# Kernel tuning notes

Hardware: AMD Instinct MI355X
Metric: run time of the kernel (lower is better)

## Reference

```python
import jax, jax.numpy as jnp
import numpy as np

MESH_SIZE = 0.01
TEMP = 0.001
T = 4096
HID = (16, 16, 16)


def _triangle_mesh():
    g = np.arange(-1.0, 1.0 + 1e-9, MESH_SIZE, dtype=np.float32)  # 201 pts
    A, B = np.meshgrid(g, g, indexing='ij')  # alpha rows, beta cols
    mask = A >= B                             # Preisach triangle alpha >= beta
    return A[mask].astype(np.float32), B[mask].astype(np.float32)  # [N], [N]


def _constrain(v, lo, hi):
    return lo + (hi - lo) * jax.nn.sigmoid(v)


def setup_inputs() -> dict:
    key = jax.random.key(0)
    ks = jax.random.split(key, 12)
    alpha_np, beta_np = _triangle_mesh()
    N = alpha_np.shape[0]  # 20301

    def xavier(k, fan_in, fan_out):
        b = np.sqrt(6.0 / (fan_in + fan_out)).astype(np.float32)
        return jax.random.uniform(k, (fan_in, fan_out), jnp.float32, -b, b)

    dims = (2,) + HID + (1,)
    params = {}
    for i in range(4):
        params[f'w{i+1}'] = xavier(ks[i], dims[i], dims[i + 1])
        params[f'b{i+1}'] = jnp.zeros((dims[i + 1],), jnp.float32)

    bound = np.sqrt(6.0 / (1 + N)).astype(np.float32)  # xavier_uniform on (1,N)
    init_state_raw = jax.random.uniform(ks[10], (N,), jnp.float32, -bound, bound)

    return dict(
        x=jax.random.normal(ks[11], (T,), jnp.float32),
        alpha_raw=jnp.asarray(alpha_np),
        beta_raw=jnp.asarray(beta_np),
        init_state_raw=init_state_raw,
        m_scale_raw=jnp.asarray(1.0, jnp.float32),
        m_offset_raw=jnp.asarray(1.0, jnp.float32),
        h_scale_raw=jnp.asarray(1.0, jnp.float32),
        **params,
    )


def _get_states(x, alpha, beta, s0, temp):
    # Soft Preisach relay: switch up where u>alpha, down where u<beta, else hold.
    def step(s, u):
        up = jax.nn.sigmoid((u - alpha) / temp)
        dn = jax.nn.sigmoid((beta - u) / temp)
        s_new = up - dn + (1.0 - up) * (1.0 - dn) * s
        return s_new, s_new
    _, states = jax.lax.scan(step, s0, x)
    return states  # [T, N]


def reference(x, alpha_raw, beta_raw, init_state_raw,
              w1, b1, w2, b2, w3, b3, w4, b4,
              m_scale_raw, m_offset_raw, h_scale_raw):
    alpha = alpha_raw  # ConstrainedParameter with no bounds -> identity
    beta = beta_raw
    s0 = jnp.tanh(init_state_raw)  # BinaryParameter (soft binary)

    states = _get_states(x, alpha, beta, s0, TEMP)  # [T, N]

    mesh = jnp.stack([alpha, beta], axis=1)  # [N, 2]
    h = jax.nn.relu(mesh @ w1 + b1)
    h = jax.nn.relu(h @ w2 + b2)
    h = jax.nn.relu(h @ w3 + b3)
    density = jax.nn.sigmoid(h @ w4 + b4)  # [N, 1]
    density = density.T  # [1, N]

    m = jnp.sum(density * states, axis=-1) / jnp.sum(density, axis=-1)  # [T]

    m_scale = _constrain(m_scale_raw, 0.0, 10.0)
    m_offset = _constrain(m_offset_raw, -10.0, 10.0)
    h_scale = _constrain(h_scale_raw, 0.0, 10.0)

    out = m_scale * m + m_offset + h_scale * x  # [T]
    return out, density, states
```

## Files before the change

kernel.cpp:

```cpp
#include <hip/hip_runtime.h>
#include <math.h>

#define NM 20301
#define TT 4096
#define NC 64
#define CH 64
#define NBLK 80
#define SBLK 20
#define NPROW (SBLK * 4)
#define TPH 16
#define NPH (CH / TPH)
#define LOG2E_K 1442.69504f
#define WNEAR 26.0f

__device__ __forceinline__ void relay_step(float ka, float kb, float ku,
                                           float& aa, float& bb) {
    float z1 = fminf(ka - ku, 63.f);
    float z2 = fminf(ku - kb, 63.f);
    float e1 = __builtin_amdgcn_exp2f(z1);
    float e2 = __builtin_amdgcn_exp2f(z2);
    float p1 = 1.f + e1, p2 = 1.f + e2;
    float r  = __builtin_amdgcn_rcpf(p1 * p2);
    aa = (e2 - e1) * r;
    bb = (e1 * e2) * r;
}

__device__ __forceinline__ float wave_reduce_sum(float w) {
    #pragma unroll
    for (int off = 32; off > 0; off >>= 1)
        w += __shfl_down(w, off, 64);
    return w;
}

__global__ __launch_bounds__(256) void density_kernel(
    const float* __restrict__ alpha, const float* __restrict__ beta,
    const float* __restrict__ w1, const float* __restrict__ b1,
    const float* __restrict__ w2, const float* __restrict__ b2,
    const float* __restrict__ w3, const float* __restrict__ b3,
    const float* __restrict__ w4, const float* __restrict__ b4,
    float* __restrict__ density_out, float* __restrict__ densum_parts)
{
    int n = blockIdx.x * 256 + threadIdx.x;
    bool valid = n < NM;
    int nn = valid ? n : NM - 1;
    float a = alpha[nn], b = beta[nn];

    float h1[16], h2[16], h3[16];
    #pragma unroll
    for (int j = 0; j < 16; j++) {
        float v = fmaf(a, w1[j], fmaf(b, w1[16 + j], b1[j]));
        h1[j] = fmaxf(v, 0.f);
    }
    #pragma unroll
    for (int j = 0; j < 16; j++) {
        float v = b2[j];
        #pragma unroll
        for (int k = 0; k < 16; k++) v = fmaf(h1[k], w2[k * 16 + j], v);
        h2[j] = fmaxf(v, 0.f);
    }
    #pragma unroll
    for (int j = 0; j < 16; j++) {
        float v = b3[j];
        #pragma unroll
        for (int k = 0; k < 16; k++) v = fmaf(h2[k], w3[k * 16 + j], v);
        h3[j] = fmaxf(v, 0.f);
    }
    float v = b4[0];
    #pragma unroll
    for (int k = 0; k < 16; k++) v = fmaf(h3[k], w4[k], v);
    float d = 1.f / (1.f + __expf(-v));

    if (valid) density_out[n] = d;
    float wsum = wave_reduce_sum(valid ? d : 0.f);
    __shared__ float ws_[4];
    if ((threadIdx.x & 63) == 0) ws_[threadIdx.x >> 6] = wsum;
    __syncthreads();
    if (threadIdx.x == 0)
        densum_parts[blockIdx.x] = ws_[0] + ws_[1] + ws_[2] + ws_[3];
}

__global__ __launch_bounds__(256) void chunk_compose_kernel(
    const float* __restrict__ x, const float* __restrict__ alpha,
    const float* __restrict__ beta,
    float* __restrict__ Abuf, float* __restrict__ Bbuf)
{
    __shared__ float xs[CH];
    int c = blockIdx.y;
    if (threadIdx.x < CH) xs[threadIdx.x] = x[c * CH + threadIdx.x] * LOG2E_K;
    __syncthreads();

    int n = blockIdx.x * 256 + threadIdx.x;
    int nn = (n < NM) ? n : NM - 1;
    float ka = alpha[nn] * LOG2E_K;
    float kb = beta[nn] * LOG2E_K;

    float A = 0.f, B = 1.f;
    for (int p = 0; p < NPH; p++) {
        float xr[TPH];
        #pragma unroll
        for (int j = 0; j < TPH; j++) xr[j] = xs[p * TPH + j];
        #pragma unroll
        for (int j = 0; j < TPH; j++) {
            float ku = xr[j];
            float d1 = ka - ku, d2 = ku - kb;
            bool nearb = fminf(fabsf(d1), fabsf(d2)) < WNEAR;
            if (__any(nearb)) {
                float aa, bb;
                relay_step(ka, kb, ku, aa, bb);
                A = fmaf(bb, A, aa);
                B *= bb;
            } else {
                bool su = d1 < 0.f, sd = d2 < 0.f;
                A = su ? 1.f : (sd ? -1.f : A);
                B = (su || sd) ? 0.f : B;
            }
        }
    }
    if (n < NM) { Abuf[(size_t)c * NM + n] = A; Bbuf[(size_t)c * NM + n] = B; }
}

__global__ __launch_bounds__(256) void chunk_scan_kernel(
    const float* __restrict__ init_raw,
    const float* __restrict__ Abuf, const float* __restrict__ Bbuf,
    float* __restrict__ sstart)
{
    int n = blockIdx.x * 256 + threadIdx.x;
    if (n >= NM) return;
    float s = tanhf(init_raw[n]);
    #pragma unroll 4
    for (int c = 0; c < NC; c++) {
        sstart[(size_t)c * NM + n] = s;
        s = fmaf(Bbuf[(size_t)c * NM + n], s, Abuf[(size_t)c * NM + n]);
    }
}

__global__ __launch_bounds__(256) void states_kernel(
    const float* __restrict__ x, const float* __restrict__ alpha,
    const float* __restrict__ beta, const float* __restrict__ density,
    const float* __restrict__ sstart,
    float* __restrict__ states, float* __restrict__ partials)
{
    __shared__ float xs[CH];
    __shared__ float tile[4 * 64 * (TPH + 1)];

    int tid = threadIdx.x;
    int c = blockIdx.y;
    if (tid < CH) xs[tid] = x[c * CH + tid] * LOG2E_K;

    int n0 = blockIdx.x * 1024 + tid;
    float s[4], d[4], ka[4], kb[4];
    bool v[4];
    #pragma unroll
    for (int q = 0; q < 4; q++) {
        int n = n0 + q * 256;
        v[q] = n < NM;
        int nn = v[q] ? n : NM - 1;
        ka[q] = alpha[nn] * LOG2E_K;
        kb[q] = beta[nn] * LOG2E_K;
        d[q]  = v[q] ? density[n] : 0.f;
        s[q]  = sstart[(size_t)c * NM + nn];
    }
    __syncthreads();

    int wv = tid >> 6, ln = tid & 63;
    int tl = ln & 15, h = ln >> 4;
    float* wtile = &tile[wv * 64 * (TPH + 1)];
    float* tslot = &wtile[ln * (TPH + 1)];
    float* rp    = states + (size_t)c * CH * NM + n0;
    size_t prow  = (size_t)(blockIdx.x * 4 + wv) * TT + c * CH;

    for (int p = 0; p < NPH; p++) {
        float xr[TPH];
        #pragma unroll
        for (int j = 0; j < TPH; j++) xr[j] = xs[p * TPH + j];
        #pragma unroll
        for (int j = 0; j < TPH; j++) {
            float u = xr[j];
            float w1_[4], w2_[4], nr[4];
            #pragma unroll
            for (int q = 0; q < 4; q++) {
                w1_[q] = ka[q] - u;
                w2_[q] = u - kb[q];
                nr[q]  = fminf(fabsf(w1_[q]), fabsf(w2_[q]));
            }
            float nmin = fminf(fminf(nr[0], nr[1]), fminf(nr[2], nr[3]));
            if (__any(nmin < WNEAR)) {
                #pragma unroll
                for (int q = 0; q < 4; q++) {
                    float aa, bb;
                    relay_step(ka[q], kb[q], u, aa, bb);
                    s[q] = fmaf(bb, s[q], aa);
                }
            } else {
                #pragma unroll
                for (int q = 0; q < 4; q++)
                    s[q] = (w1_[q] < 0.f) ? 1.f
                         : ((w2_[q] < 0.f) ? -1.f : s[q]);
            }
            #pragma unroll
            for (int q = 0; q < 4; q++)
                if (v[q]) rp[q * 256] = s[q];
            rp += NM;
            tslot[j] = fmaf(d[0], s[0], fmaf(d[1], s[1],
                       fmaf(d[2], s[2], d[3] * s[3])));
        }
        asm volatile("s_waitcnt lgkmcnt(0)" ::: "memory");
        float acc = 0.f;
        #pragma unroll
        for (int k = 0; k < TPH; k++)
            acc += wtile[(h * 16 + k) * (TPH + 1) + tl];
        acc += __shfl_xor(acc, 16, 64);
        acc += __shfl_xor(acc, 32, 64);
        if (ln < TPH) partials[prow + p * TPH + ln] = acc;
        asm volatile("s_waitcnt lgkmcnt(0)" ::: "memory");
    }
}

__global__ __launch_bounds__(256) void finalize_kernel(
    const float* __restrict__ x, const float* __restrict__ partials,
    const float* __restrict__ densum_parts,
    const float* __restrict__ msr, const float* __restrict__ mor,
    const float* __restrict__ hsr, float* __restrict__ out)
{
    int t = blockIdx.x * 256 + threadIdx.x;
    if (t >= TT) return;
    float acc = 0.f;
    for (int r = 0; r < NPROW; r++)
        acc += partials[(size_t)r * TT + t];
    float dsum = 0.f;
    for (int bx = 0; bx < NBLK; bx++)
        dsum += densum_parts[bx];
    float sig_ms = 1.f / (1.f + __expf(-msr[0]));
    float sig_mo = 1.f / (1.f + __expf(-mor[0]));
    float sig_hs = 1.f / (1.f + __expf(-hsr[0]));
    float m_scale  = 10.f * sig_ms;
    float m_offset = fmaf(20.f, sig_mo, -10.f);
    float h_scale  = 10.f * sig_hs;
    float m = acc / dsum;
    out[t] = fmaf(m_scale, m, m_offset) + h_scale * x[t];
}

extern "C" void kernel_launch(void* const* d_in, const int* in_sizes, int n_in,
                              void* d_out, int out_size, void* d_ws, size_t ws_size,
                              hipStream_t stream)
{
    const float* x    = (const float*)d_in[0];
    const float* alpha= (const float*)d_in[1];
    const float* beta = (const float*)d_in[2];
    const float* init = (const float*)d_in[3];
    const float* msr  = (const float*)d_in[4];
    const float* mor  = (const float*)d_in[5];
    const float* hsr  = (const float*)d_in[6];
    const float* w1   = (const float*)d_in[7];
    const float* b1   = (const float*)d_in[8];
    const float* w2   = (const float*)d_in[9];
    const float* b2   = (const float*)d_in[10];
    const float* w3   = (const float*)d_in[11];
    const float* b3   = (const float*)d_in[12];
    const float* w4   = (const float*)d_in[13];
    const float* b4   = (const float*)d_in[14];

    float* out     = (float*)d_out;
    float* density = out + TT;
    float* states  = density + NM;

    float* densum_parts = (float*)d_ws;
    float* sstart       = densum_parts + 128;
    float* partials     = sstart + (size_t)NC * NM;

    float* Abuf = states;
    float* Bbuf = states + (size_t)NC * NM;

    density_kernel<<<dim3(NBLK), dim3(256), 0, stream>>>(
        alpha, beta, w1, b1, w2, b2, w3, b3, w4, b4, density, densum_parts);

    chunk_compose_kernel<<<dim3(NBLK, NC), dim3(256), 0, stream>>>(
        x, alpha, beta, Abuf, Bbuf);

    chunk_scan_kernel<<<dim3(NBLK), dim3(256), 0, stream>>>(
        init, Abuf, Bbuf, sstart);

    states_kernel<<<dim3(SBLK, NC), dim3(256), 0, stream>>>(
        x, alpha, beta, density, sstart, states, partials);

    finalize_kernel<<<dim3(TT / 256), dim3(256), 0, stream>>>(
        x, partials, densum_parts, msr, mor, hsr, out);
}
```

Before: 452.9 us.

## Fuse chunk compose, scan and states into one decoupled-lookback kernel

Replaces the three-pass chunked scan (compose, sequential chunk scan, states replay) with a single kernel. Each block first computes its chunk's affine composition assuming a zero start and writes those provisional states. It then publishes A/B via release flags and looks back over earlier chunks, stopping early once the composed multiplier becomes zero. A final fix-up pass rewrites states only while the start state still matters and adds density-weighted corrections into an extra partials row. This removes one full relay-step pass over all timesteps and the sstart round trip. In exchange it adds spin-waiting on inter-block flags, with a recompute fallback after a timeout, plus extra shared-memory atomics.

```diff
diff --git a/kernel.cpp b/kernel.cpp
--- a/kernel.cpp
+++ b/kernel.cpp
@@ -8,8 +8,10 @@
 #define NBLK 80
 #define SBLK 20
 #define NPROW (SBLK * 4)
+#define NROWS (NPROW + SBLK)
 #define TPH 16
 #define NPH (CH / TPH)
+#define NFLAGS (NC * SBLK)
 #define LOG2E_K 1442.69504f
 #define WNEAR 26.0f
 
@@ -38,9 +40,11 @@
     const float* __restrict__ w2, const float* __restrict__ b2,
     const float* __restrict__ w3, const float* __restrict__ b3,
     const float* __restrict__ w4, const float* __restrict__ b4,
-    float* __restrict__ density_out, float* __restrict__ densum_parts)
+    float* __restrict__ density_out, float* __restrict__ densum_parts,
+    int* __restrict__ flags)
 {
     int n = blockIdx.x * 256 + threadIdx.x;
+    if (n < NFLAGS) flags[n] = 0;
     bool valid = n < NM;
     int nn = valid ? n : NM - 1;
     float a = alpha[nn], b = beta[nn];
@@ -79,76 +83,24 @@
         densum_parts[blockIdx.x] = ws_[0] + ws_[1] + ws_[2] + ws_[3];
 }
 
-__global__ __launch_bounds__(256) void chunk_compose_kernel(
-    const float* __restrict__ x, const float* __restrict__ alpha,
-    const float* __restrict__ beta,
-    float* __restrict__ Abuf, float* __restrict__ Bbuf)
-{
-    __shared__ float xs[CH];
-    int c = blockIdx.y;
-    if (threadIdx.x < CH) xs[threadIdx.x] = x[c * CH + threadIdx.x] * LOG2E_K;
-    __syncthreads();
-
-    int n = blockIdx.x * 256 + threadIdx.x;
-    int nn = (n < NM) ? n : NM - 1;
-    float ka = alpha[nn] * LOG2E_K;
-    float kb = beta[nn] * LOG2E_K;
-
-    float A = 0.f, B = 1.f;
-    for (int p = 0; p < NPH; p++) {
-        float xr[TPH];
-        #pragma unroll
-        for (int j = 0; j < TPH; j++) xr[j] = xs[p * TPH + j];
-        #pragma unroll
-        for (int j = 0; j < TPH; j++) {
-            float ku = xr[j];
-            float d1 = ka - ku, d2 = ku - kb;
-            bool nearb = fminf(fabsf(d1), fabsf(d2)) < WNEAR;
-            if (__any(nearb)) {
-                float aa, bb;
-                relay_step(ka, kb, ku, aa, bb);
-                A = fmaf(bb, A, aa);
-                B *= bb;
-            } else {
-                bool su = d1 < 0.f, sd = d2 < 0.f;
-                A = su ? 1.f : (sd ? -1.f : A);
-                B = (su || sd) ? 0.f : B;
-            }
-        }
-    }
-    if (n < NM) { Abuf[(size_t)c * NM + n] = A; Bbuf[(size_t)c * NM + n] = B; }
-}
-
-__global__ __launch_bounds__(256) void chunk_scan_kernel(
-    const float* __restrict__ init_raw,
-    const float* __restrict__ Abuf, const float* __restrict__ Bbuf,
-    float* __restrict__ sstart)
-{
-    int n = blockIdx.x * 256 + threadIdx.x;
-    if (n >= NM) return;
-    float s = tanhf(init_raw[n]);
-    #pragma unroll 4
-    for (int c = 0; c < NC; c++) {
-        sstart[(size_t)c * NM + n] = s;
-        s = fmaf(Bbuf[(size_t)c * NM + n], s, Abuf[(size_t)c * NM + n]);
-    }
-}
-
-__global__ __launch_bounds__(256) void states_kernel(
+__global__ __launch_bounds__(256) void states_fused_kernel(
     const float* __restrict__ x, const float* __restrict__ alpha,
     const float* __restrict__ beta, const float* __restrict__ density,
-    const float* __restrict__ sstart,
+    const float* __restrict__ init_raw,
+    float* __restrict__ Acomp, float* __restrict__ Bcomp,
+    int* __restrict__ flags,
     float* __restrict__ states, float* __restrict__ partials)
 {
     __shared__ float xs[CH];
     __shared__ float tile[4 * 64 * (TPH + 1)];
+    __shared__ float dl[CH];
 
     int tid = threadIdx.x;
-    int c = blockIdx.y;
-    if (tid < CH) xs[tid] = x[c * CH + tid] * LOG2E_K;
-
-    int n0 = blockIdx.x * 1024 + tid;
-    float s[4], d[4], ka[4], kb[4];
+    int c = blockIdx.y, bx = blockIdx.x;
+    if (tid < CH) { xs[tid] = x[c * CH + tid] * LOG2E_K; dl[tid] = 0.f; }
+
+    int n0 = bx * 1024 + tid;
+    float A[4], B[4], d[4], ka[4], kb[4], s0[4];
     bool v[4];
     #pragma unroll
     for (int q = 0; q < 4; q++) {
@@ -158,7 +110,8 @@
         ka[q] = alpha[nn] * LOG2E_K;
         kb[q] = beta[nn] * LOG2E_K;
         d[q]  = v[q] ? density[n] : 0.f;
-        s[q]  = sstart[(size_t)c * NM + nn];
+        s0[q] = tanhf(init_raw[nn]);
+        A[q] = 0.f; B[q] = 1.f;
     }
     __syncthreads();
 
@@ -167,7 +120,7 @@
     float* wtile = &tile[wv * 64 * (TPH + 1)];
     float* tslot = &wtile[ln * (TPH + 1)];
     float* rp    = states + (size_t)c * CH * NM + n0;
-    size_t prow  = (size_t)(blockIdx.x * 4 + wv) * TT + c * CH;
+    size_t prow  = (size_t)(bx * 4 + wv) * TT + c * CH;
 
     for (int p = 0; p < NPH; p++) {
         float xr[TPH];
@@ -176,33 +129,25 @@
         #pragma unroll
         for (int j = 0; j < TPH; j++) {
             float u = xr[j];
-            float w1_[4], w2_[4], nr[4];
             #pragma unroll
             for (int q = 0; q < 4; q++) {
-                w1_[q] = ka[q] - u;
-                w2_[q] = u - kb[q];
-                nr[q]  = fminf(fabsf(w1_[q]), fabsf(w2_[q]));
-            }
-            float nmin = fminf(fminf(nr[0], nr[1]), fminf(nr[2], nr[3]));
-            if (__any(nmin < WNEAR)) {
-                #pragma unroll
-                for (int q = 0; q < 4; q++) {
+                float d1 = ka[q] - u, d2 = u - kb[q];
+                float nr = fminf(fabsf(d1), fabsf(d2));
+                if (__any(nr < WNEAR)) {
                     float aa, bb;
                     relay_step(ka[q], kb[q], u, aa, bb);
-                    s[q] = fmaf(bb, s[q], aa);
+                    A[q] = fmaf(bb, A[q], aa);
+                    B[q] *= bb;
+                } else {
+                    bool su = d1 < 0.f, sd = d2 < 0.f;
+                    A[q] = su ? 1.f : (sd ? -1.f : A[q]);
+                    B[q] = (su || sd) ? 0.f : B[q];
                 }
-            } else {
-                #pragma unroll
-                for (int q = 0; q < 4; q++)
-                    s[q] = (w1_[q] < 0.f) ? 1.f
-                         : ((w2_[q] < 0.f) ? -1.f : s[q]);
+                if (v[q]) rp[q * 256] = A[q];
             }
-            #pragma unroll
-            for (int q = 0; q < 4; q++)
-                if (v[q]) rp[q * 256] = s[q];
             rp += NM;
-            tslot[j] = fmaf(d[0], s[0], fmaf(d[1], s[1],
-                       fmaf(d[2], s[2], d[3] * s[3])));
+            tslot[j] = fmaf(d[0], A[0], fmaf(d[1], A[1],
+                       fmaf(d[2], A[2], d[3] * A[3])));
         }
         asm volatile("s_waitcnt lgkmcnt(0)" ::: "memory");
         float acc = 0.f;
@@ -214,6 +159,98 @@
         if (ln < TPH) partials[prow + p * TPH + ln] = acc;
         asm volatile("s_waitcnt lgkmcnt(0)" ::: "memory");
     }
+
+    #pragma unroll
+    for (int q = 0; q < 4; q++) {
+        if (v[q]) {
+            Acomp[(size_t)c * NM + n0 + q * 256] = A[q];
+            Bcomp[(size_t)c * NM + n0 + q * 256] = B[q];
+        }
+    }
+    __threadfence();
+    __syncthreads();
+    if (tid == 0)
+        __hip_atomic_store(&flags[c * SBLK + bx], 1,
+                           __ATOMIC_RELEASE, __HIP_MEMORY_SCOPE_AGENT);
+
+    float P[4] = {0.f, 0.f, 0.f, 0.f}, Q[4] = {1.f, 1.f, 1.f, 1.f};
+    for (int k = c - 1; k >= 0; --k) {
+        bool need = (Q[0] != 0.f) | (Q[1] != 0.f) | (Q[2] != 0.f) | (Q[3] != 0.f);
+        if (!__any(need)) break;
+        float Ak[4], Bk[4];
+        int spins = 0; bool have = false;
+        while (!have) {
+            if (__hip_atomic_load(&flags[k * SBLK + bx],
+                                  __ATOMIC_ACQUIRE, __HIP_MEMORY_SCOPE_AGENT)) {
+                #pragma unroll
+                for (int q = 0; q < 4; q++) {
+                    int nn = v[q] ? n0 + q * 256 : NM - 1;
+                    Ak[q] = Acomp[(size_t)k * NM + nn];
+                    Bk[q] = Bcomp[(size_t)k * NM + nn];
+                }
+                have = true;
+            } else if (++spins > (1 << 16)) {
+                #pragma unroll
+                for (int q = 0; q < 4; q++) { Ak[q] = 0.f; Bk[q] = 1.f; }
+                #pragma unroll 1
+                for (int j = 0; j < CH; j++) {
+                    float u = x[k * CH + j] * LOG2E_K;
+                    #pragma unroll
+                    for (int q = 0; q < 4; q++) {
+                        float aa, bb;
+                        relay_step(ka[q], kb[q], u, aa, bb);
+                        Ak[q] = fmaf(bb, Ak[q], aa);
+                        Bk[q] *= bb;
+                    }
+                }
+                have = true;
+            } else {
+                __builtin_amdgcn_s_sleep(2);
+            }
+        }
+        #pragma unroll
+        for (int q = 0; q < 4; q++) {
+            P[q] = fmaf(Q[q], Ak[q], P[q]);
+            Q[q] *= Bk[q];
+        }
+    }
+    float ss[4];
+    #pragma unroll
+    for (int q = 0; q < 4; q++) ss[q] = fmaf(Q[q], s0[q], P[q]);
+
+    float Af[4] = {0.f, 0.f, 0.f, 0.f}, Bf[4] = {1.f, 1.f, 1.f, 1.f};
+    float* rp2 = states + (size_t)c * CH * NM + n0;
+    #pragma unroll 1
+    for (int j = 0; j < CH; j++) {
+        bool live = (Bf[0] != 0.f) | (Bf[1] != 0.f) | (Bf[2] != 0.f) | (Bf[3] != 0.f);
+        if (!__any(live)) break;
+        float u = xs[j];
+        #pragma unroll
+        for (int q = 0; q < 4; q++) {
+            float d1 = ka[q] - u, d2 = u - kb[q];
+            float nr = fminf(fabsf(d1), fabsf(d2));
+            if (__any(nr < WNEAR)) {
+                float aa, bb;
+                relay_step(ka[q], kb[q], u, aa, bb);
+                Af[q] = fmaf(bb, Af[q], aa);
+                Bf[q] *= bb;
+                ss[q] = fmaf(bb, ss[q], aa);
+            } else {
+                bool su = d1 < 0.f, sd = d2 < 0.f;
+                Af[q] = su ? 1.f : (sd ? -1.f : Af[q]);
+                ss[q] = su ? 1.f : (sd ? -1.f : ss[q]);
+                Bf[q] = (su || sd) ? 0.f : Bf[q];
+            }
+            if (Bf[q] != 0.f && v[q]) {
+                rp2[q * 256] = ss[q];
+                atomicAdd(&dl[j], d[q] * (ss[q] - Af[q]));
+            }
+        }
+        rp2 += NM;
+    }
+    __syncthreads();
+    if (tid < CH)
+        partials[(size_t)(NPROW + bx) * TT + c * CH + tid] = dl[tid];
 }
 
 __global__ __launch_bounds__(256) void finalize_kernel(
@@ -225,7 +262,7 @@
     int t = blockIdx.x * 256 + threadIdx.x;
     if (t >= TT) return;
     float acc = 0.f;
-    for (int r = 0; r < NPROW; r++)
+    for (int r = 0; r < NROWS; r++)
         acc += partials[(size_t)r * TT + t];
     float dsum = 0.f;
     for (int bx = 0; bx < NBLK; bx++)
@@ -265,23 +302,17 @@
     float* states  = density + NM;
 
     float* densum_parts = (float*)d_ws;
-    float* sstart       = densum_parts + 128;
-    float* partials     = sstart + (size_t)NC * NM;
-
-    float* Abuf = states;
-    float* Bbuf = states + (size_t)NC * NM;
+    float* partials     = densum_parts + 128;
+    int*   flags        = (int*)(partials + (size_t)NROWS * TT);
+    float* Acomp        = (float*)(flags + 2048);
+    float* Bcomp        = Acomp + (size_t)NC * NM;
 
     density_kernel<<<dim3(NBLK), dim3(256), 0, stream>>>(
-        alpha, beta, w1, b1, w2, b2, w3, b3, w4, b4, density, densum_parts);
-
-    chunk_compose_kernel<<<dim3(NBLK, NC), dim3(256), 0, stream>>>(
-        x, alpha, beta, Abuf, Bbuf);
-
-    chunk_scan_kernel<<<dim3(NBLK), dim3(256), 0, stream>>>(
-        init, Abuf, Bbuf, sstart);
-
-    states_kernel<<<dim3(SBLK, NC), dim3(256), 0, stream>>>(
-        x, alpha, beta, density, sstart, states, partials);
+        alpha, beta, w1, b1, w2, b2, w3, b3, w4, b4,
+        density, densum_parts, flags);
+
+    states_fused_kernel<<<dim3(SBLK, NC), dim3(256), 0, stream>>>(
+        x, alpha, beta, density, init, Acomp, Bcomp, flags, states, partials);
 
     finalize_kernel<<<dim3(TT / 256), dim3(256), 0, stream>>>(
         x, partials, densum_parts, msr, mor, hsr, out);
```

Measured after the change: 785.8 us. 1.74x slower.

## Speculate chunk states from zero start and fix up with sequential correction pass

Applied to the files above, without the earlier changes.

Replaces the compose/scan/states pipeline with a speculative states pass that assumes each chunk starts at A=0 and writes A as the state while also recording the chunk composition (A,B). A fixup kernel then scans chunk starts sequentially and, per chunk, re-runs steps only while the carried multiplier B is nonzero. It patches those states and atomically adds density-weighted corrections to the per-time sums. This drops one full relay-evaluation pass over all chunks and the start-state round trip. The cost is a long sequential fixup kernel with per-step wave reductions and atomics, which is only cheap if the relay saturates early in each chunk.

```diff
diff --git a/kernel.cpp b/kernel.cpp
--- a/kernel.cpp
+++ b/kernel.cpp
@@ -38,9 +38,11 @@
     const float* __restrict__ w2, const float* __restrict__ b2,
     const float* __restrict__ w3, const float* __restrict__ b3,
     const float* __restrict__ w4, const float* __restrict__ b4,
-    float* __restrict__ density_out, float* __restrict__ densum_parts)
+    float* __restrict__ density_out, float* __restrict__ densum_parts,
+    float* __restrict__ corr)
 {
     int n = blockIdx.x * 256 + threadIdx.x;
+    if (n < TT) corr[n] = 0.f;
     bool valid = n < NM;
     int nn = valid ? n : NM - 1;
     float a = alpha[nn], b = beta[nn];
@@ -79,66 +81,11 @@
         densum_parts[blockIdx.x] = ws_[0] + ws_[1] + ws_[2] + ws_[3];
 }
 
-__global__ __launch_bounds__(256) void chunk_compose_kernel(
-    const float* __restrict__ x, const float* __restrict__ alpha,
-    const float* __restrict__ beta,
-    float* __restrict__ Abuf, float* __restrict__ Bbuf)
-{
-    __shared__ float xs[CH];
-    int c = blockIdx.y;
-    if (threadIdx.x < CH) xs[threadIdx.x] = x[c * CH + threadIdx.x] * LOG2E_K;
-    __syncthreads();
-
-    int n = blockIdx.x * 256 + threadIdx.x;
-    int nn = (n < NM) ? n : NM - 1;
-    float ka = alpha[nn] * LOG2E_K;
-    float kb = beta[nn] * LOG2E_K;
-
-    float A = 0.f, B = 1.f;
-    for (int p = 0; p < NPH; p++) {
-        float xr[TPH];
-        #pragma unroll
-        for (int j = 0; j < TPH; j++) xr[j] = xs[p * TPH + j];
-        #pragma unroll
-        for (int j = 0; j < TPH; j++) {
-            float ku = xr[j];
-            float d1 = ka - ku, d2 = ku - kb;
-            bool nearb = fminf(fabsf(d1), fabsf(d2)) < WNEAR;
-            if (__any(nearb)) {
-                float aa, bb;
-                relay_step(ka, kb, ku, aa, bb);
-                A = fmaf(bb, A, aa);
-                B *= bb;
-            } else {
-                bool su = d1 < 0.f, sd = d2 < 0.f;
-                A = su ? 1.f : (sd ? -1.f : A);
-                B = (su || sd) ? 0.f : B;
-            }
-        }
-    }
-    if (n < NM) { Abuf[(size_t)c * NM + n] = A; Bbuf[(size_t)c * NM + n] = B; }
-}
-
-__global__ __launch_bounds__(256) void chunk_scan_kernel(
-    const float* __restrict__ init_raw,
-    const float* __restrict__ Abuf, const float* __restrict__ Bbuf,
-    float* __restrict__ sstart)
-{
-    int n = blockIdx.x * 256 + threadIdx.x;
-    if (n >= NM) return;
-    float s = tanhf(init_raw[n]);
-    #pragma unroll 4
-    for (int c = 0; c < NC; c++) {
-        sstart[(size_t)c * NM + n] = s;
-        s = fmaf(Bbuf[(size_t)c * NM + n], s, Abuf[(size_t)c * NM + n]);
-    }
-}
-
-__global__ __launch_bounds__(256) void states_kernel(
+__global__ __launch_bounds__(256) void states_spec_kernel(
     const float* __restrict__ x, const float* __restrict__ alpha,
     const float* __restrict__ beta, const float* __restrict__ density,
-    const float* __restrict__ sstart,
-    float* __restrict__ states, float* __restrict__ partials)
+    float* __restrict__ states, float* __restrict__ partials,
+    float* __restrict__ Acomp, float* __restrict__ Bcomp)
 {
     __shared__ float xs[CH];
     __shared__ float tile[4 * 64 * (TPH + 1)];
@@ -148,7 +95,7 @@
     if (tid < CH) xs[tid] = x[c * CH + tid] * LOG2E_K;
 
     int n0 = blockIdx.x * 1024 + tid;
-    float s[4], d[4], ka[4], kb[4];
+    float A[4], B[4], d[4], ka[4], kb[4];
     bool v[4];
     #pragma unroll
     for (int q = 0; q < 4; q++) {
@@ -158,7 +105,7 @@
         ka[q] = alpha[nn] * LOG2E_K;
         kb[q] = beta[nn] * LOG2E_K;
         d[q]  = v[q] ? density[n] : 0.f;
-        s[q]  = sstart[(size_t)c * NM + nn];
+        A[q] = 0.f; B[q] = 1.f;
     }
     __syncthreads();
 
@@ -189,20 +136,23 @@
                 for (int q = 0; q < 4; q++) {
                     float aa, bb;
                     relay_step(ka[q], kb[q], u, aa, bb);
-                    s[q] = fmaf(bb, s[q], aa);
+                    A[q] = fmaf(bb, A[q], aa);
+                    B[q] *= bb;
                 }
             } else {
                 #pragma unroll
-                for (int q = 0; q < 4; q++)
-                    s[q] = (w1_[q] < 0.f) ? 1.f
-                         : ((w2_[q] < 0.f) ? -1.f : s[q]);
+                for (int q = 0; q < 4; q++) {
+                    bool su = w1_[q] < 0.f, sd = w2_[q] < 0.f;
+                    A[q] = su ? 1.f : (sd ? -1.f : A[q]);
+                    B[q] = (su || sd) ? 0.f : B[q];
+                }
             }
             #pragma unroll
             for (int q = 0; q < 4; q++)
-                if (v[q]) rp[q * 256] = s[q];
+                if (v[q]) rp[q * 256] = A[q];
             rp += NM;
-            tslot[j] = fmaf(d[0], s[0], fmaf(d[1], s[1],
-                       fmaf(d[2], s[2], d[3] * s[3])));
+            tslot[j] = fmaf(d[0], A[0], fmaf(d[1], A[1],
+                       fmaf(d[2], A[2], d[3] * A[3])));
         }
         asm volatile("s_waitcnt lgkmcnt(0)" ::: "memory");
         float acc = 0.f;
@@ -214,17 +164,73 @@
         if (ln < TPH) partials[prow + p * TPH + ln] = acc;
         asm volatile("s_waitcnt lgkmcnt(0)" ::: "memory");
     }
+
+    #pragma unroll
+    for (int q = 0; q < 4; q++) {
+        if (v[q]) {
+            Acomp[(size_t)c * NM + n0 + q * 256] = A[q];
+            Bcomp[(size_t)c * NM + n0 + q * 256] = B[q];
+        }
+    }
+}
+
+__global__ __launch_bounds__(256) void fixup_kernel(
+    const float* __restrict__ x, const float* __restrict__ alpha,
+    const float* __restrict__ beta, const float* __restrict__ density,
+    const float* __restrict__ init_raw,
+    const float* __restrict__ Acomp, const float* __restrict__ Bcomp,
+    float* __restrict__ states, float* __restrict__ corr)
+{
+    __shared__ float xs[TT];
+    int tid = threadIdx.x;
+    for (int i = tid; i < TT; i += 256) xs[i] = x[i] * LOG2E_K;
+
+    int n = blockIdx.x * 256 + tid;
+    bool valid = n < NM;
+    int nn = valid ? n : NM - 1;
+    float ka = alpha[nn] * LOG2E_K;
+    float kb = beta[nn] * LOG2E_K;
+    float d  = valid ? density[n] : 0.f;
+    float s  = tanhf(init_raw[nn]);
+    __syncthreads();
+
+    int ln = tid & 63;
+    float An = Acomp[nn], Bn = Bcomp[nn];
+    for (int c = 0; c < NC; c++) {
+        float Ac = An, Bc = Bn;
+        if (c + 1 < NC) {
+            An = Acomp[(size_t)(c + 1) * NM + nn];
+            Bn = Bcomp[(size_t)(c + 1) * NM + nn];
+        }
+        float Bf = 1.f;
+        float ss = s;
+        float* rp = states + (size_t)c * CH * NM + n;
+        #pragma unroll 1
+        for (int j = 0; j < CH; j++) {
+            if (!__any(Bf != 0.f)) break;
+            float u = xs[c * CH + j];
+            float aa, bb;
+            relay_step(ka, kb, u, aa, bb);
+            Bf *= bb;
+            ss = fmaf(bb, ss, aa);
+            if (valid && Bf != 0.f) rp[0] = ss;
+            float contrib = wave_reduce_sum(d * Bf * s);
+            if (ln == 0 && contrib != 0.f) atomicAdd(&corr[c * CH + j], contrib);
+            rp += NM;
+        }
+        s = fmaf(Bc, s, Ac);
+    }
 }
 
 __global__ __launch_bounds__(256) void finalize_kernel(
     const float* __restrict__ x, const float* __restrict__ partials,
-    const float* __restrict__ densum_parts,
+    const float* __restrict__ corr, const float* __restrict__ densum_parts,
     const float* __restrict__ msr, const float* __restrict__ mor,
     const float* __restrict__ hsr, float* __restrict__ out)
 {
     int t = blockIdx.x * 256 + threadIdx.x;
     if (t >= TT) return;
-    float acc = 0.f;
+    float acc = corr[t];
     for (int r = 0; r < NPROW; r++)
         acc += partials[(size_t)r * TT + t];
     float dsum = 0.f;
@@ -265,24 +271,21 @@
     float* states  = density + NM;
 
     float* densum_parts = (float*)d_ws;
-    float* sstart       = densum_parts + 128;
-    float* partials     = sstart + (size_t)NC * NM;
-
-    float* Abuf = states;
-    float* Bbuf = states + (size_t)NC * NM;
+    float* corr         = densum_parts + 128;
+    float* partials     = corr + TT;
+    float* Acomp        = partials + (size_t)NPROW * TT;
+    float* Bcomp        = Acomp + (size_t)NC * NM;
 
     density_kernel<<<dim3(NBLK), dim3(256), 0, stream>>>(
-        alpha, beta, w1, b1, w2, b2, w3, b3, w4, b4, density, densum_parts);
-
-    chunk_compose_kernel<<<dim3(NBLK, NC), dim3(256), 0, stream>>>(
-        x, alpha, beta, Abuf, Bbuf);
-
-    chunk_scan_kernel<<<dim3(NBLK), dim3(256), 0, stream>>>(
-        init, Abuf, Bbuf, sstart);
-
-    states_kernel<<<dim3(SBLK, NC), dim3(256), 0, stream>>>(
-        x, alpha, beta, density, sstart, states, partials);
+        alpha, beta, w1, b1, w2, b2, w3, b3, w4, b4,
+        density, densum_parts, corr);
+
+    states_spec_kernel<<<dim3(SBLK, NC), dim3(256), 0, stream>>>(
+        x, alpha, beta, density, states, partials, Acomp, Bcomp);
+
+    fixup_kernel<<<dim3(NBLK), dim3(256), 0, stream>>>(
+        x, alpha, beta, density, init, Acomp, Bcomp, states, corr);
 
     finalize_kernel<<<dim3(TT / 256), dim3(256), 0, stream>>>(
-        x, partials, densum_parts, msr, mor, hsr, out);
-}
+        x, partials, corr, densum_parts, msr, mor, hsr, out);
+}
```

Measured after the change: 538.3 us. 18.9% more time.
